# Performance work log

Measured on AMD Instinct MI355X. Metric: run time of the kernel, lower is better.

## Reference

```python
import jax, jax.numpy as jnp
import numpy as np

B = 8192
D = 4096  # input_size == hidden_size (required by the module's forward)
H = 4096


def setup_inputs() -> dict:
    key = jax.random.key(0)
    ks = jax.random.split(key, 14)
    s = 0.02
    inp = {
        "input": jax.random.normal(ks[0], (B, D), dtype=jnp.float32),
        "hidden_state": jax.random.normal(ks[1], (B, H), dtype=jnp.float32),
        # torch nn.Linear weights: [out_features, in_features]
        "w_ir": jax.random.normal(ks[2], (H, D), dtype=jnp.float32) * s,
        "b_ir": jax.random.normal(ks[3], (H,), dtype=jnp.float32) * s,
        "w_iz": jax.random.normal(ks[4], (H, D), dtype=jnp.float32) * s,
        "b_iz": jax.random.normal(ks[5], (H,), dtype=jnp.float32) * s,
        "w_in": jax.random.normal(ks[6], (H, D), dtype=jnp.float32) * s,
        "b_in": jax.random.normal(ks[7], (H,), dtype=jnp.float32) * s,
        "w_hr": jax.random.normal(ks[8], (H, H), dtype=jnp.float32) * s,
        "b_hr": jax.random.normal(ks[9], (H,), dtype=jnp.float32) * s,
        "w_hz": jax.random.normal(ks[10], (H, H), dtype=jnp.float32) * s,
        "b_hz": jax.random.normal(ks[11], (H,), dtype=jnp.float32) * s,
        "w_hn": jax.random.normal(ks[12], (H, H), dtype=jnp.float32) * s,
        "b_hn": jax.random.normal(ks[13], (H,), dtype=jnp.float32) * s,
    }
    return inp


def reference(input, hidden_state, w_ir, b_ir, w_iz, b_iz, w_in, b_in,
              w_hr, b_hr, w_hz, b_hz, w_hn, b_hn):
    # NOTE: faithful to the source: ALL six gates are applied to `input`
    # (the hidden_* gates are also fed `input`, not hidden_state), and the
    # "new" gate uses sigmoid (not tanh).
    # Fuse the six small GEMMs into one batched GEMM: stack weights [6H, D].
    W = jnp.concatenate([w_ir, w_iz, w_in, w_hr, w_hz, w_hn], axis=0)  # [6H, D]
    bvec = jnp.concatenate([b_ir, b_iz, b_in, b_hr, b_hz, b_hn], axis=0)  # [6H]
    g = jnp.einsum('bd,od->bo', input, W) + bvec  # [B, 6H]
    ir, iz, inn, hr, hz, hn = jnp.split(g, 6, axis=-1)
    r = jax.nn.sigmoid(ir + hr)
    z = jax.nn.sigmoid(iz + hz)
    n = jax.nn.sigmoid(inn + r * hn)
    return (1.0 - z) * hidden_state + z * n
```

## Files before the change

kernel.cpp:

```cpp
#include <hip/hip_runtime.h>
#include <hip/hip_bf16.h>


#define B_DIM 8192
#define D_DIM 4096
#define H_DIM 4096
#define BM 128
#define GBN 64
#define BK 32
#define NT (D_DIM / BK)
#define TBYTES 24576

#define WS_WR 0
#define WS_WZ 33554432
#define WS_WN 67108864
#define WS_WH 100663296
#define WS_A  134217728
#define WS_NEED 201326592ULL

typedef __attribute__((ext_vector_type(8))) short bf16x8;
typedef __attribute__((ext_vector_type(4))) float f32x4;
typedef __attribute__((ext_vector_type(4))) int i32x4;

__device__ __forceinline__ unsigned f2bf(float f) {
    union { float f; unsigned u; } v; v.f = f;
    return (v.u + 0x7FFFu + ((v.u >> 16) & 1u)) >> 16;
}
__device__ __forceinline__ unsigned pk(float a, float b) {
    return (f2bf(a) & 0xFFFFu) | (f2bf(b) << 16);
}
__device__ __forceinline__ i32x4 pack8(float4 x, float4 y) {
    i32x4 r;
    r[0] = (int)pk(x.x, x.y); r[1] = (int)pk(x.z, x.w);
    r[2] = (int)pk(y.x, y.y); r[3] = (int)pk(y.z, y.w);
    return r;
}
__device__ __forceinline__ float sigmoidf_(float x) {
    return 1.0f / (1.0f + __expf(-x));
}
__device__ __forceinline__ void gld16(const void* g, void* l) {
    __builtin_amdgcn_global_load_lds(
        (const __attribute__((address_space(1))) unsigned*)g,
        (__attribute__((address_space(3))) unsigned*)l, 16, 0, 0);
}

__global__ __launch_bounds__(256) void prep_w_t(
    const float* __restrict__ ir, const float* __restrict__ hr,
    const float* __restrict__ iz, const float* __restrict__ hz,
    const float* __restrict__ inw, const float* __restrict__ hn,
    char* __restrict__ wsbase)
{
    const int tx = threadIdx.x;
    const int R = tx & 15;
    const int c8loc = tx >> 4;
    const int bx = blockIdx.x;
    const int c8blk = bx & 31;
    const int hgrp = bx >> 5;
    const int gy = blockIdx.y;
    const int h  = hgrp * 16 + R;
    const int c8 = c8blk * 16 + c8loc;

    const float* s1 = (gy == 0) ? ir : (gy == 1) ? iz : (gy == 2) ? inw : hn;
    const size_t fi = ((size_t)h * 512 + c8) * 2;
    const float4* p1 = (const float4*)s1;
    float4 a0 = p1[fi], a1 = p1[fi + 1];
    if (gy < 2) {
        const float4* p2 = (const float4*)((gy == 0) ? hr : hz);
        a0 = a0 + p2[fi];
        a1 = a1 + p2[fi + 1];
    }
    const i32x4 v = pack8(a0, a1);
    const int hblk = h >> 6, nfr = (h >> 4) & 3;
    const int t = c8 >> 2, C = c8 & 3;
    const size_t addr = (size_t)gy * 33554432 + (size_t)hblk * 524288
                      + (size_t)t * 4096 + nfr * 1024 + C * 256 + R * 16;
    *(i32x4*)(wsbase + addr) = v;
}

__global__ __launch_bounds__(256) void prep_a_t(const float* __restrict__ in,
                                                char* __restrict__ abase)
{
    const int tx = threadIdx.x;
    const int R = tx & 15;
    const int c8loc = tx >> 4;
    const int bx = blockIdx.x;
    const int c8blk = bx & 31;
    const int bgrp = bx >> 5;
    const int b  = bgrp * 16 + R;
    const int c8 = c8blk * 16 + c8loc;

    const size_t fi = ((size_t)b * 512 + c8) * 2;
    const float4* p = (const float4*)in;
    const i32x4 v = pack8(p[fi], p[fi + 1]);
    const int bblk = b >> 7, mfr = (b >> 4) & 7;
    const int t = c8 >> 2, C = c8 & 3;
    const size_t addr = (size_t)bblk * 1048576 + (size_t)t * 8192
                      + mfr * 1024 + C * 256 + R * 16;
    *(i32x4*)(abase + addr) = v;
}

__global__ __launch_bounds__(256, 2) void gru_bf16(
    const char* __restrict__ Abf, const char* __restrict__ Wr,
    const char* __restrict__ Wz, const char* __restrict__ Wn,
    const char* __restrict__ Wh,
    const float* __restrict__ hidden,
    const float* __restrict__ b_ir, const float* __restrict__ b_iz,
    const float* __restrict__ b_in, const float* __restrict__ b_hr,
    const float* __restrict__ b_hz, const float* __restrict__ b_hn,
    float* __restrict__ out)
{
    __shared__ __attribute__((aligned(128))) char smem[2 * TBYTES];

    const int tid  = threadIdx.x;
    const int lane = tid & 63;
    const int wid  = tid >> 6;
    const int wn   = wid;

    const int nb   = (int)blockIdx.x;
    const int bblk = nb & 63;
    const int hblk = nb >> 6;
    const int b0 = bblk * BM;
    const int h0 = hblk * GBN;

    const char* sp[6];  int lo[6];  int kst[6];
#pragma unroll
    for (int i = 0; i < 6; ++i) {
        const int f = wid * 6 + i;
        if (f < 8) {
            sp[i]  = Abf + (size_t)bblk * 1048576 + f * 1024;
            lo[i]  = f * 1024;
            kst[i] = 8192;
        } else {
            const int bf = f - 8, g = bf >> 2, nf = bf & 3;
            const char* W = (g == 0) ? Wr : (g == 1) ? Wz : (g == 2) ? Wn : Wh;
            sp[i]  = W + (size_t)hblk * 524288 + nf * 1024;
            lo[i]  = 8192 + g * 4096 + nf * 1024;
            kst[i] = 4096;
        }
        sp[i] += (size_t)lane * 16;
    }
    const char* rp[6];
#pragma unroll
    for (int i = 0; i < 6; ++i) rp[i] = sp[i] + kst[i];

    f32x4 acc[4][8];
#pragma unroll
    for (int g = 0; g < 4; ++g)
#pragma unroll
        for (int m = 0; m < 8; ++m) acc[g][m] = (f32x4)0.0f;

#define MM(acc_, a_, b_) acc_ = __builtin_amdgcn_mfma_f32_16x16x32_bf16(a_, b_, acc_, 0, 0, 0)

#pragma unroll
    for (int i = 0; i < 6; ++i) gld16(sp[i], smem + lo[i]);
    asm volatile("s_waitcnt vmcnt(0)" ::: "memory");
    __builtin_amdgcn_sched_barrier(0);
    __builtin_amdgcn_s_barrier();

#pragma unroll 1
    for (int t = 0; t < NT; ++t) {
        const char* cb = smem + (t & 1) * TBYTES;
        char* d = smem + ((t + 1) & 1) * TBYTES;
        const bool stg = (t + 1 < NT);

        if (stg) {
#pragma unroll
            for (int i = 0; i < 6; ++i) {
                gld16(rp[i], d + lo[i]);
                rp[i] += kst[i];
            }
        }
        bf16x8 af[8], fb[4];
#pragma unroll
        for (int mf = 0; mf < 8; ++mf)
            af[mf] = *(const bf16x8*)(cb + mf * 1024 + (lane << 4));
#pragma unroll
        for (int g = 0; g < 4; ++g)
            fb[g] = *(const bf16x8*)(cb + 8192 + g * 4096 + wn * 1024 + (lane << 4));

        __builtin_amdgcn_s_setprio(1);
#pragma unroll
        for (int g = 0; g < 4; ++g)
#pragma unroll
            for (int mf = 0; mf < 8; ++mf)
                MM(acc[g][mf], af[mf], fb[g]);
        __builtin_amdgcn_s_setprio(0);

        if (stg) { asm volatile("s_waitcnt vmcnt(0)" ::: "memory"); }
        __builtin_amdgcn_sched_barrier(0);
        __builtin_amdgcn_s_barrier();
    }

    const int r4 = (lane >> 4) * 4;
    const int cn = lane & 15;
    {
        const int h = h0 + wn * 16 + cn;
        const float br = b_ir[h] + b_hr[h];
        const float bz = b_iz[h] + b_hz[h];
        const float bn = b_in[h];
        const float bh = b_hn[h];
#pragma unroll
        for (int m = 0; m < 8; ++m) {
            const int brow = b0 + m * 16 + r4;
#pragma unroll
            for (int j = 0; j < 4; ++j) {
                const size_t idx = (size_t)(brow + j) * H_DIM + h;
                const float r = sigmoidf_(acc[0][m][j] + br);
                const float z = sigmoidf_(acc[1][m][j] + bz);
                const float n = sigmoidf_(acc[2][m][j] + bn + r * (acc[3][m][j] + bh));
                out[idx] = (1.0f - z) * hidden[idx] + z * n;
            }
        }
    }
#undef MM
}

__global__ __launch_bounds__(512, 2) void gru_fused_f32(
    const float* __restrict__ input, const float* __restrict__ hidden,
    const float* __restrict__ w_ir, const float* __restrict__ b_ir,
    const float* __restrict__ w_iz, const float* __restrict__ b_iz,
    const float* __restrict__ w_in, const float* __restrict__ b_in,
    const float* __restrict__ w_hr, const float* __restrict__ b_hr,
    const float* __restrict__ w_hz, const float* __restrict__ b_hz,
    const float* __restrict__ w_hn, const float* __restrict__ b_hn,
    float* __restrict__ out)
{
    __shared__ int smem[2 * 10240];
    const int tid  = threadIdx.x;
    const int lane = tid & 63;
    const int wid  = tid >> 6;
    const int wm   = wid >> 2;
    const int wn   = wid & 3;
    const int bblk = blockIdx.x & 63;
    const int hblk = blockIdx.x >> 6;
    const int b0 = bblk * 128;
    const int h0 = hblk * 128;
    const int srow = tid >> 2;
    const int sc   = tid & 3;
    const float4* gA  = (const float4*)(input + (size_t)(b0 + srow) * D_DIM + sc * 8);
    const size_t woff = (size_t)(h0 + srow) * D_DIM + sc * 8;
    const float4* gIr = (const float4*)(w_ir + woff);
    const float4* gHr = (const float4*)(w_hr + woff);
    const float4* gIz = (const float4*)(w_iz + woff);
    const float4* gHz = (const float4*)(w_hz + woff);
    const float4* gIn = (const float4*)(w_in + woff);
    const float4* gHn = (const float4*)(w_hn + woff);
    const int wr_ints = (srow >> 4) * 256 + ((sc * 16 + (srow & 15)) * 4);

    f32x4 accR[4][2], accZ[4][2], accN[4][2], accH[4][2];
#pragma unroll
    for (int mf = 0; mf < 4; ++mf)
#pragma unroll
        for (int nf = 0; nf < 2; ++nf) {
            accR[mf][nf] = (f32x4)0.0f; accZ[mf][nf] = (f32x4)0.0f;
            accN[mf][nf] = (f32x4)0.0f; accH[mf][nf] = (f32x4)0.0f;
        }
    float4 La0, La1, Lr0, Lr1, Lr2, Lr3, Lz0, Lz1, Lz2, Lz3, Ln0, Ln1, Lh0, Lh1;
#define LOADREGS(s) do { const int o = (s) * 8;                          \
        La0 = gA[o];  La1 = gA[o + 1];                                   \
        Lr0 = gIr[o]; Lr1 = gIr[o + 1]; Lr2 = gHr[o]; Lr3 = gHr[o + 1];  \
        Lz0 = gIz[o]; Lz1 = gIz[o + 1]; Lz2 = gHz[o]; Lz3 = gHz[o + 1];  \
        Ln0 = gIn[o]; Ln1 = gIn[o + 1];                                  \
        Lh0 = gHn[o]; Lh1 = gHn[o + 1]; } while (0)
#define WRITELDS(pp) do { const int wb = (pp) * 10240 + wr_ints;          \
        *(i32x4*)&smem[wb]        = pack8(La0, La1);                      \
        *(i32x4*)&smem[wb + 2048] = pack8(Lr0 + Lr2, Lr1 + Lr3);          \
        *(i32x4*)&smem[wb + 4096] = pack8(Lz0 + Lz2, Lz1 + Lz3);          \
        *(i32x4*)&smem[wb + 6144] = pack8(Ln0, Ln1);                      \
        *(i32x4*)&smem[wb + 8192] = pack8(Lh0, Lh1); } while (0)
#define COMPUTE(pp) do {                                                  \
        const int cb = (pp) * 10240;                                      \
        const bf16x8* Af = (const bf16x8*)&smem[cb];                      \
        const bf16x8* Br = (const bf16x8*)&smem[cb + 2048];               \
        const bf16x8* Bz = (const bf16x8*)&smem[cb + 4096];               \
        const bf16x8* Bn = (const bf16x8*)&smem[cb + 6144];               \
        const bf16x8* Bh = (const bf16x8*)&smem[cb + 8192];               \
        bf16x8 afr[4];                                                    \
        _Pragma("unroll")                                                 \
        for (int mf = 0; mf < 4; ++mf)                                    \
            afr[mf] = Af[(wm * 4 + mf) * 64 + lane];                      \
        _Pragma("unroll")                                                 \
        for (int nf = 0; nf < 2; ++nf) {                                  \
            const int bi = (wn * 2 + nf) * 64 + lane;                     \
            bf16x8 fr = Br[bi], fz = Bz[bi], fn = Bn[bi], fh = Bh[bi];    \
            _Pragma("unroll")                                             \
            for (int mf = 0; mf < 4; ++mf) {                              \
                accR[mf][nf] = __builtin_amdgcn_mfma_f32_16x16x32_bf16(afr[mf], fr, accR[mf][nf], 0, 0, 0); \
                accZ[mf][nf] = __builtin_amdgcn_mfma_f32_16x16x32_bf16(afr[mf], fz, accZ[mf][nf], 0, 0, 0); \
                accN[mf][nf] = __builtin_amdgcn_mfma_f32_16x16x32_bf16(afr[mf], fn, accN[mf][nf], 0, 0, 0); \
                accH[mf][nf] = __builtin_amdgcn_mfma_f32_16x16x32_bf16(afr[mf], fh, accH[mf][nf], 0, 0, 0); \
            }                                                             \
        } } while (0)
    LOADREGS(0);
    WRITELDS(0);
    __syncthreads();
#pragma unroll 1
    for (int s = 0; s < 128; ++s) {
        if (s + 1 < 128) LOADREGS(s + 1);
        COMPUTE(s & 1);
        if (s + 1 < 128) { WRITELDS((s + 1) & 1); __syncthreads(); }
    }
    const int r4 = (lane >> 4) * 4;
    const int cn = lane & 15;
#pragma unroll
    for (int nf = 0; nf < 2; ++nf) {
        const int h = h0 + wn * 32 + nf * 16 + cn;
        const float br = b_ir[h] + b_hr[h];
        const float bz = b_iz[h] + b_hz[h];
        const float bn = b_in[h];
        const float bh = b_hn[h];
#pragma unroll
        for (int mf = 0; mf < 4; ++mf) {
            const int brow = b0 + wm * 64 + mf * 16 + r4;
#pragma unroll
            for (int j = 0; j < 4; ++j) {
                const size_t idx = (size_t)(brow + j) * H_DIM + h;
                const float r = sigmoidf_(accR[mf][nf][j] + br);
                const float z = sigmoidf_(accZ[mf][nf][j] + bz);
                const float n = sigmoidf_(accN[mf][nf][j] + bn + r * (accH[mf][nf][j] + bh));
                out[idx] = (1.0f - z) * hidden[idx] + z * n;
            }
        }
    }
#undef LOADREGS
#undef WRITELDS
#undef COMPUTE
}

extern "C" void kernel_launch(void* const* d_in, const int* in_sizes, int n_in,
                              void* d_out, int out_size, void* d_ws, size_t ws_size,
                              hipStream_t stream) {
    const float* input  = (const float*)d_in[0];
    const float* hidden = (const float*)d_in[1];
    const float* w_ir = (const float*)d_in[2];  const float* b_ir = (const float*)d_in[3];
    const float* w_iz = (const float*)d_in[4];  const float* b_iz = (const float*)d_in[5];
    const float* w_in = (const float*)d_in[6];  const float* b_in = (const float*)d_in[7];
    const float* w_hr = (const float*)d_in[8];  const float* b_hr = (const float*)d_in[9];
    const float* w_hz = (const float*)d_in[10]; const float* b_hz = (const float*)d_in[11];
    const float* w_hn = (const float*)d_in[12]; const float* b_hn = (const float*)d_in[13];
    float* out = (float*)d_out;

    if (ws_size >= WS_NEED) {
        char* ws = (char*)d_ws;
        prep_w_t<<<dim3(8192, 4), dim3(256), 0, stream>>>(
            w_ir, w_hr, w_iz, w_hz, w_in, w_hn, ws);
        prep_a_t<<<dim3(16384), dim3(256), 0, stream>>>(input, ws + WS_A);
        gru_bf16<<<dim3((B_DIM / BM) * (H_DIM / GBN)), dim3(256), 0, stream>>>(
            ws + WS_A, ws + WS_WR, ws + WS_WZ, ws + WS_WN, ws + WS_WH,
            hidden, b_ir, b_iz, b_in, b_hr, b_hz, b_hn, out);
    } else {
        gru_fused_f32<<<dim3(2048), dim3(512), 0, stream>>>(
            input, hidden, w_ir, b_ir, w_iz, b_iz, w_in, b_in,
            w_hr, b_hr, w_hz, b_hz, w_hn, b_hn, out);
    }
}
```

Baseline: 1.051 ms.

## Enlarge batch tile to 256 with 2x2 warp grid and 4-stage LDS pipeline

Doubles the M tile of the bf16 GRU GEMM from 128 to 256 rows and lays the four warps out as 2x2, so each warp computes 128 rows by 2 column fragments across all four gates. This doubles per-warp accumulators and cuts redundant weight loads per output. The single-stage double buffer becomes a 4-slot ring with loads issued two iterations ahead and partial vmcnt waits to hide global latency. The A prep layout is changed to match. In exchange, accumulator register use grows to 256 floats per lane, launch bounds drop to one block per CU, and LDS use rises to 128 KB, which lowers occupancy.

```diff
diff --git a/kernel.cpp b/kernel.cpp
--- a/kernel.cpp
+++ b/kernel.cpp
@@ -5,11 +5,11 @@
 #define B_DIM 8192
 #define D_DIM 4096
 #define H_DIM 4096
-#define BM 128
+#define BM 256
 #define GBN 64
 #define BK 32
 #define NT (D_DIM / BK)
-#define TBYTES 24576
+#define TBYTES 32768
 
 #define WS_WR 0
 #define WS_WZ 33554432
@@ -92,14 +92,14 @@
     const size_t fi = ((size_t)b * 512 + c8) * 2;
     const float4* p = (const float4*)in;
     const i32x4 v = pack8(p[fi], p[fi + 1]);
-    const int bblk = b >> 7, mfr = (b >> 4) & 7;
+    const int bblk = b >> 8, mfr = (b >> 4) & 15;
     const int t = c8 >> 2, C = c8 & 3;
-    const size_t addr = (size_t)bblk * 1048576 + (size_t)t * 8192
+    const size_t addr = (size_t)bblk * 2097152 + (size_t)t * 16384
                       + mfr * 1024 + C * 256 + R * 16;
     *(i32x4*)(abase + addr) = v;
 }
 
-__global__ __launch_bounds__(256, 2) void gru_bf16(
+__global__ __launch_bounds__(256, 1) void gru_bf16(
     const char* __restrict__ Abf, const char* __restrict__ Wr,
     const char* __restrict__ Wz, const char* __restrict__ Wn,
     const char* __restrict__ Wh,
@@ -109,109 +109,106 @@
     const float* __restrict__ b_hz, const float* __restrict__ b_hn,
     float* __restrict__ out)
 {
-    __shared__ __attribute__((aligned(128))) char smem[2 * TBYTES];
+    __shared__ __attribute__((aligned(128))) char smem[4 * TBYTES];
 
     const int tid  = threadIdx.x;
     const int lane = tid & 63;
     const int wid  = tid >> 6;
-    const int wn   = wid;
+    const int wm   = wid >> 1;
+    const int wq   = wid & 1;
 
     const int nb   = (int)blockIdx.x;
-    const int bblk = nb & 63;
-    const int hblk = nb >> 6;
+    const int bblk = nb & 31;
+    const int hblk = nb >> 5;
     const int b0 = bblk * BM;
     const int h0 = hblk * GBN;
 
-    const char* sp[6];  int lo[6];  int kst[6];
-#pragma unroll
-    for (int i = 0; i < 6; ++i) {
-        const int f = wid * 6 + i;
-        if (f < 8) {
-            sp[i]  = Abf + (size_t)bblk * 1048576 + f * 1024;
-            lo[i]  = f * 1024;
-            kst[i] = 8192;
-        } else {
-            const int bf = f - 8, g = bf >> 2, nf = bf & 3;
-            const char* W = (g == 0) ? Wr : (g == 1) ? Wz : (g == 2) ? Wn : Wh;
-            sp[i]  = W + (size_t)hblk * 524288 + nf * 1024;
-            lo[i]  = 8192 + g * 4096 + nf * 1024;
-            kst[i] = 4096;
-        }
-        sp[i] += (size_t)lane * 16;
-    }
-    const char* rp[6];
-#pragma unroll
-    for (int i = 0; i < 6; ++i) rp[i] = sp[i] + kst[i];
-
-    f32x4 acc[4][8];
+    const char* gW = (wid == 0) ? Wr : (wid == 1) ? Wz : (wid == 2) ? Wn : Wh;
+    const char* pA = Abf + (size_t)bblk * 2097152 + (size_t)(4 * wid) * 1024 + (lane << 4);
+    const char* pB = gW + (size_t)hblk * 524288 + (lane << 4);
+    const int dA = (4 * wid) * 1024;
+    const int dB = 16384 + wid * 4096;
+
+    f32x4 acc[4][2][8];
 #pragma unroll
     for (int g = 0; g < 4; ++g)
 #pragma unroll
-        for (int m = 0; m < 8; ++m) acc[g][m] = (f32x4)0.0f;
+        for (int nf = 0; nf < 2; ++nf)
+#pragma unroll
+            for (int mf = 0; mf < 8; ++mf) acc[g][nf][mf] = (f32x4)0.0f;
+
+#define STAGE(x) do {                                                          \
+        char* L = smem + ((x) & 3) * TBYTES;                                   \
+        const char* a_ = pA + (size_t)(x) * 16384;                             \
+        const char* b_ = pB + (size_t)(x) * 4096;                              \
+        gld16(a_, L + dA);              gld16(a_ + 1024, L + dA + 1024);       \
+        gld16(a_ + 2048, L + dA + 2048); gld16(a_ + 3072, L + dA + 3072);      \
+        gld16(b_, L + dB);              gld16(b_ + 1024, L + dB + 1024);       \
+        gld16(b_ + 2048, L + dB + 2048); gld16(b_ + 3072, L + dB + 3072);      \
+    } while (0)
 
 #define MM(acc_, a_, b_) acc_ = __builtin_amdgcn_mfma_f32_16x16x32_bf16(a_, b_, acc_, 0, 0, 0)
 
-#pragma unroll
-    for (int i = 0; i < 6; ++i) gld16(sp[i], smem + lo[i]);
-    asm volatile("s_waitcnt vmcnt(0)" ::: "memory");
+    STAGE(0);
+    STAGE(1);
+    asm volatile("s_waitcnt vmcnt(8)" ::: "memory");
     __builtin_amdgcn_sched_barrier(0);
     __builtin_amdgcn_s_barrier();
 
 #pragma unroll 1
     for (int t = 0; t < NT; ++t) {
-        const char* cb = smem + (t & 1) * TBYTES;
-        char* d = smem + ((t + 1) & 1) * TBYTES;
-        const bool stg = (t + 1 < NT);
-
-        if (stg) {
-#pragma unroll
-            for (int i = 0; i < 6; ++i) {
-                gld16(rp[i], d + lo[i]);
-                rp[i] += kst[i];
-            }
-        }
-        bf16x8 af[8], fb[4];
+        const char* cb = smem + (t & 3) * TBYTES;
+        if (t + 2 < NT) STAGE(t + 2);
+
+        bf16x8 af[8], fb[4][2];
 #pragma unroll
         for (int mf = 0; mf < 8; ++mf)
-            af[mf] = *(const bf16x8*)(cb + mf * 1024 + (lane << 4));
+            af[mf] = *(const bf16x8*)(cb + (wm * 8 + mf) * 1024 + (lane << 4));
 #pragma unroll
         for (int g = 0; g < 4; ++g)
-            fb[g] = *(const bf16x8*)(cb + 8192 + g * 4096 + wn * 1024 + (lane << 4));
+#pragma unroll
+            for (int nf = 0; nf < 2; ++nf)
+                fb[g][nf] = *(const bf16x8*)(cb + 16384 + g * 4096 + (wq * 2 + nf) * 1024 + (lane << 4));
 
         __builtin_amdgcn_s_setprio(1);
 #pragma unroll
         for (int g = 0; g < 4; ++g)
 #pragma unroll
-            for (int mf = 0; mf < 8; ++mf)
-                MM(acc[g][mf], af[mf], fb[g]);
+            for (int nf = 0; nf < 2; ++nf)
+#pragma unroll
+                for (int mf = 0; mf < 8; ++mf)
+                    MM(acc[g][nf][mf], af[mf], fb[g][nf]);
         __builtin_amdgcn_s_setprio(0);
 
-        if (stg) { asm volatile("s_waitcnt vmcnt(0)" ::: "memory"); }
+        if (t + 2 < NT) { asm volatile("s_waitcnt vmcnt(8)" ::: "memory"); }
+        else            { asm volatile("s_waitcnt vmcnt(0)" ::: "memory"); }
         __builtin_amdgcn_sched_barrier(0);
         __builtin_amdgcn_s_barrier();
     }
 
     const int r4 = (lane >> 4) * 4;
     const int cn = lane & 15;
-    {
-        const int h = h0 + wn * 16 + cn;
+#pragma unroll
+    for (int nf = 0; nf < 2; ++nf) {
+        const int h = h0 + wq * 32 + nf * 16 + cn;
         const float br = b_ir[h] + b_hr[h];
         const float bz = b_iz[h] + b_hz[h];
         const float bn = b_in[h];
         const float bh = b_hn[h];
 #pragma unroll
-        for (int m = 0; m < 8; ++m) {
-            const int brow = b0 + m * 16 + r4;
+        for (int mf = 0; mf < 8; ++mf) {
+            const int brow = b0 + wm * 128 + mf * 16 + r4;
 #pragma unroll
             for (int j = 0; j < 4; ++j) {
                 const size_t idx = (size_t)(brow + j) * H_DIM + h;
-                const float r = sigmoidf_(acc[0][m][j] + br);
-                const float z = sigmoidf_(acc[1][m][j] + bz);
-                const float n = sigmoidf_(acc[2][m][j] + bn + r * (acc[3][m][j] + bh));
+                const float r = sigmoidf_(acc[0][nf][mf][j] + br);
+                const float z = sigmoidf_(acc[1][nf][mf][j] + bz);
+                const float n = sigmoidf_(acc[2][nf][mf][j] + bn + r * (acc[3][nf][mf][j] + bh));
                 out[idx] = (1.0f - z) * hidden[idx] + z * n;
             }
         }
     }
+#undef STAGE
 #undef MM
 }
 
```

After: 1.494 ms. 1.42x slower.
